# Kernel tuning notes

Measured on AMD Instinct MI355X. Metric: run time of the kernel, lower is better.

The kernel has to match this reference:

```python
import jax, jax.numpy as jnp
import numpy as np

B, T, H, IN = 256, 1024, 512, 1

def setup_inputs() -> dict:
    key = jax.random.key(0)
    ks = jax.random.split(key, 10)
    s = 1.0 / np.sqrt(H)
    return {
        "input": jax.random.normal(ks[0], (B, T), dtype=jnp.float32),
        "Wx0": jax.random.uniform(ks[1], (IN, 4 * H), jnp.float32, -s, s),
        "Wh0": jax.random.uniform(ks[2], (H, 4 * H), jnp.float32, -s, s),
        "b0": jax.random.uniform(ks[3], (4 * H,), jnp.float32, -s, s),
        "Wx1": jax.random.uniform(ks[4], (H, 4 * H), jnp.float32, -s, s),
        "Wh1": jax.random.uniform(ks[5], (H, 4 * H), jnp.float32, -s, s),
        "b1": jax.random.uniform(ks[6], (4 * H,), jnp.float32, -s, s),
        "Wf": jax.random.uniform(ks[7], (H, 1), jnp.float32, -s, s),
        "bf": jax.random.uniform(ks[8], (1,), jnp.float32, -s, s),
    }

def _lstm_layer(xs, Wx, Wh, b):
    # xs: [T, B, in] -> hs: [T, B, H]
    Bd = xs.shape[1]
    Hd = Wh.shape[0]
    h0 = jnp.zeros((Bd, Hd), xs.dtype)
    c0 = jnp.zeros((Bd, Hd), xs.dtype)
    def step(carry, x_t):
        h, c = carry
        g = x_t @ Wx + h @ Wh + b                     # [B, 4H]
        i, f, gg, o = jnp.split(g, 4, axis=-1)
        i = jax.nn.sigmoid(i)
        f = jax.nn.sigmoid(f)
        gg = jnp.tanh(gg)
        o = jax.nn.sigmoid(o)
        c_n = f * c + i * gg
        h_n = o * jnp.tanh(c_n)
        return (h_n, c_n), h_n
    _, hs = jax.lax.scan(step, (h0, c0), xs)
    return hs

def reference(input, Wx0, Wh0, b0, Wx1, Wh1, b1, Wf, bf):
    # input: [B, T] scalar sequence (input_size = 1)
    xs = input.T[:, :, None]                           # [T, B, 1]
    h1 = _lstm_layer(xs, Wx0, Wh0, b0)                 # [T, B, H]
    h2 = _lstm_layer(h1, Wx1, Wh1, b1)                 # [T, B, H]
    out = h2 @ Wf + bf                                 # [T, B, 1]
    return out[:, :, 0].T                              # [B, T]
```

## Files before the change

### kernel.cpp

```cpp
#include <hip/hip_runtime.h>


typedef _Float16 f16;
typedef _Float16 f16x8 __attribute__((ext_vector_type(8)));
typedef float f32x4 __attribute__((ext_vector_type(4)));
typedef unsigned long long u64;

#define NB 256
#define NT_ 1024
#define NH 512
#define RING 16
#define SLOT (NB * NH)

__device__ __forceinline__ float sigm(float x)  { return 1.0f / (1.0f + __expf(-x)); }
__device__ __forceinline__ float tanhx(float x) { return 2.0f / (1.0f + __expf(-2.0f * x)) - 1.0f; }

__device__ __forceinline__ void st8(unsigned short* p, u64 v) {
  __hip_atomic_store((u64*)p, v, __ATOMIC_RELAXED, __HIP_MEMORY_SCOPE_AGENT);
}
__device__ __forceinline__ void stf(unsigned* p, unsigned v) {
  __hip_atomic_store(p, v, __ATOMIC_RELAXED, __HIP_MEMORY_SCOPE_AGENT);
}
__device__ __forceinline__ unsigned ldf(const unsigned* p) {
  return __hip_atomic_load(p, __ATOMIC_RELAXED, __HIP_MEMORY_SCOPE_AGENT);
}
__device__ __forceinline__ unsigned pollr(const unsigned* a, unsigned thr) {
  unsigned v;
  for (;;) {
    v = ldf(a);
    if (!~__ballot(v >= thr)) break;
    __builtin_amdgcn_s_sleep(1);
  }
  asm volatile("" ::: "memory");
  return v;
}

__device__ __forceinline__ unsigned* PFL(unsigned* pf, int c, int j, int r) {
  return pf + (((c * 32 + j) * 4) + r) * 32;
}
__device__ __forceinline__ unsigned* QFL(unsigned* qf, int c, int j, int r) {
  return qf + (((c * 32 + j) * 4) + r) * 32;
}

__global__ void prep_xT(const float* __restrict__ inp, float* __restrict__ xT) {
  int g = blockIdx.x * 256 + threadIdx.x;
  int t = g >> 8, b = g & 255;
  xT[t * NB + b] = inp[b * NT_ + t];
}

__global__ void prep_w(const float* __restrict__ Wh0,
                       const float* __restrict__ Wx1,
                       const float* __restrict__ Wh1,
                       f16* __restrict__ dst) {
  int g = blockIdx.x * 256 + threadIdx.x;
  int mat = g >> 20;
  int r = g & 0xFFFFF;
  int j = r & 7, ln = (r >> 3) & 63, kt = (r >> 9) & 15;
  int cl = ln & 15, qd = ln >> 4;
  int k = kt * 32 + qd * 8 + j;
  int jt = (r >> 13) & 1, nh = (r >> 14) & 1, sl = (r >> 15) & 31;
  const float* W = (mat == 0) ? Wh0 : (mat == 1) ? Wx1 : Wh1;
  int gate = jt * 2 + (cl >> 3);
  int gcol = gate * 512 + sl * 16 + nh * 8 + (cl & 7);
  size_t di = (size_t)mat * 1048576 + (size_t)sl * 32768 +
              (((size_t)(nh * 2 + jt) * 16 + kt) * 64 + ln) * 8 + j;
  dst[di] = (f16)W[(size_t)k * 2048 + gcol];
}

__global__ void reduce_out(const float* __restrict__ part8,
                           const float* __restrict__ bfp,
                           float* __restrict__ out) {
  int g = blockIdx.x * 256 + threadIdx.x;
  float v = bfp[0];
#pragma unroll
  for (int j = 0; j < 8; ++j) v += part8[(size_t)j * (NB * NT_) + g];
  out[g] = v;
}

__global__ __launch_bounds__(256, 1) void lstm_main(
    const float* __restrict__ xT,
    const f16*  __restrict__ wsl,
    const float* __restrict__ wx0,
    const float* __restrict__ bias0,
    const float* __restrict__ bias1,
    const float* __restrict__ wf,
    unsigned short* p_hi, unsigned short* p_lo,
    unsigned short* q_hi, unsigned short* q_lo,
    unsigned int* pf,
    unsigned int* qf,
    float* part8)
{
  extern __shared__ char smem[];
  const int tid = threadIdx.x;
  const int wv = tid >> 6, ln = tid & 63;
  const int qd = ln >> 4, cl = ln & 15;
  const int bx = blockIdx.x;
  const int r8 = bx & 7, idx = bx >> 3;
  const bool isL0 = !(r8 & 1);
  const int c = r8 >> 1;
  const int sl = idx;
  const float LO = 1.0f / 1024.0f;
  const int u = cl & 7, g01 = cl >> 3;
  const bool hiH = (cl < 8);
  const int lr = wv * 16 + cl;

  if (isL0) {
    const int4* s0 = (const int4*)wsl + (size_t)sl * 4096;
    int4* d = (int4*)smem;
    for (int i = tid; i < 4096; i += 256) d[i] = s0[i];
  } else {
    const int4* s1 = (const int4*)wsl + 131072 + (size_t)sl * 4096;
    const int4* s2 = (const int4*)wsl + 262144 + (size_t)sl * 4096;
    int4* d = (int4*)smem;
    for (int i = tid; i < 4096; i += 256) { d[i] = s1[i]; d[4096 + i] = s2[i]; }
  }
  __syncthreads();

  if (isL0) {
    float w0a[2], w0b[2], b0a[2], b0b[2];
#pragma unroll
    for (int nh = 0; nh < 2; ++nh) {
      int base = sl * 16 + nh * 8 + u;
      w0a[nh] = wx0[g01 * 512 + base];
      b0a[nh] = bias0[g01 * 512 + base];
      w0b[nh] = wx0[(2 + g01) * 512 + base];
      b0b[nh] = bias0[(2 + g01) * 512 + base];
    }
    float cst[2][4] = {{0.f,0.f,0.f,0.f},{0.f,0.f,0.f,0.f}};
    const unsigned* pwa = (ln < 32) ? PFL(pf, c, ln, sl & 3)
                                    : QFL(qf, c, ln - 32, sl & 3);
    const f16x8* wl = (const f16x8*)smem;
    f16* sh  = (f16*)(smem + 65536);
    f16* slo = sh + 1024;

    for (int s = 0; s < NT_; ++s) {
      if ((s & (RING - 1)) == 0 && s) {
        __syncthreads();
        if (wv == 0)
          asm volatile("buffer_inv sc1\n\ts_waitcnt vmcnt(0)" ::: "memory");
        __syncthreads();
      }
      const int slot_r = (s + RING - 1) & (RING - 1);
      const int slot_w = s & (RING - 1);
      float4 xv = *(const float4*)(xT + s * NB + c * 64 + wv * 16 + qd * 4);
      if (s) {
        unsigned thr = (ln < 32) ? (unsigned)s
                                 : (s >= RING ? (unsigned)(s - RING + 1) : 0u);
        pollr(pwa, thr);
      }
      const f16* ah = (const f16*)p_hi + (size_t)slot_r * SLOT + (size_t)c * 32768 +
                      (qd >> 1) * 1024 + lr * 16 + (qd & 1) * 8;
      const f16* al = (const f16*)p_lo + (size_t)slot_r * SLOT + (size_t)c * 32768 +
                      (qd >> 1) * 1024 + lr * 16 + (qd & 1) * 8;
      f16x8 Ah[16], Al[16];
#pragma unroll
      for (int kt = 0; kt < 16; ++kt) {
        Ah[kt] = *(const f16x8*)(ah + kt * 2048);
        Al[kt] = *(const f16x8*)(al + kt * 2048);
      }
      f32x4 acc[4], accL[4];
#pragma unroll
      for (int t4 = 0; t4 < 4; ++t4) {
        acc[t4] = (f32x4){0.f,0.f,0.f,0.f};
        accL[t4] = (f32x4){0.f,0.f,0.f,0.f};
      }
#pragma unroll
      for (int kt = 0; kt < 16; ++kt) {
#pragma unroll
        for (int t4 = 0; t4 < 4; ++t4) {
          f16x8 bw = wl[(t4 * 16 + kt) * 64 + ln];
          acc[t4]  = __builtin_amdgcn_mfma_f32_16x16x32_f16(Ah[kt], bw, acc[t4], 0, 0, 0);
          accL[t4] = __builtin_amdgcn_mfma_f32_16x16x32_f16(Al[kt], bw, accL[t4], 0, 0, 0);
        }
      }
#pragma unroll
      for (int e = 0; e < 4; ++e) {
        float xe = (e == 0) ? xv.x : (e == 1) ? xv.y : (e == 2) ? xv.z : xv.w;
        int r = wv * 16 + qd * 4 + e;
#pragma unroll
        for (int nh = 0; nh < 2; ++nh) {
          float v0 = acc[nh*2+0][e] + accL[nh*2+0][e] * LO + xe * w0a[nh] + b0a[nh];
          float v1 = acc[nh*2+1][e] + accL[nh*2+1][e] * LO + xe * w0b[nh] + b0b[nh];
          float w0 = __shfl_xor(v0, 8, 16);
          float w1 = __shfl_xor(v1, 8, 16);
          float gi = hiH ? v0 : w0;
          float gf = hiH ? w0 : v0;
          float gg = hiH ? v1 : w1;
          float go = hiH ? w1 : v1;
          float ii = sigm(gi), ff = sigm(gf), tg = tanhx(gg), oo = sigm(go);
          cst[nh][e] = ff * cst[nh][e] + ii * tg;
          float h = oo * tanhx(cst[nh][e]);
          int su = r * 16 + nh * 8 + u;
          if (hiH) {
            sh[su] = (f16)h;
          } else {
            f16 hh = (f16)h;
            slo[su] = (f16)((h - (float)hh) * 1024.0f);
          }
        }
      }
      __syncthreads();
      {
        unsigned short* bh = p_hi + (size_t)slot_w * SLOT + (size_t)c * 32768 + (size_t)sl * 1024;
        unsigned short* bl = p_lo + (size_t)slot_w * SLOT + (size_t)c * 32768 + (size_t)sl * 1024;
#pragma unroll
        for (int i = tid; i < 512; i += 256) {
          int strm = i >> 8, pc = i & 255;
          const f16* src = (strm ? slo : sh) + pc * 4;
          st8((strm ? bl : bh) + pc * 4, *(const u64*)src);
        }
      }
      __syncthreads();
      if (tid < 4)
        stf(PFL(pf, c, sl, tid), (unsigned)(s + 1));
    }
  } else {
    float b1c0[2], b1c1[2], wfv[2];
#pragma unroll
    for (int nh = 0; nh < 2; ++nh) {
      int base = sl * 16 + nh * 8 + u;
      b1c0[nh] = bias1[g01 * 512 + base];
      b1c1[nh] = bias1[(2 + g01) * 512 + base];
      wfv[nh] = wf[base];
    }
    float cst[2][4] = {{0.f,0.f,0.f,0.f},{0.f,0.f,0.f,0.f}};
    const unsigned* a_init = (ln < 32) ? QFL(qf, c, ln, sl & 3)
                                       : PFL(pf, c, ln - 32, sl & 3);
    const unsigned* ppf = PFL(pf, c, ln & 31, (sl + (ln >> 5)) & 3);
    const f16x8* wx_ = (const f16x8*)smem;
    const f16x8* wh_ = (const f16x8*)(smem + 65536);
    f16* sh  = (f16*)(smem + 131072);
    f16* slo = sh + 1024;

    for (int s = 0; s < NT_; ++s) {
      if ((s & (RING - 1)) == 0 && s) {
        __syncthreads();
        if (wv == 0)
          asm volatile("buffer_inv sc1\n\ts_waitcnt vmcnt(0)" ::: "memory");
        __syncthreads();
      }
      const int slot_r = (s + RING - 1) & (RING - 1);
      const int slot_w = s & (RING - 1);
      bool early = false;
      if (s) {
        unsigned thr_i = (ln < 32) ? (unsigned)s : (unsigned)(s + 1);
        unsigned v = ldf(a_init);
        u64 bal = __ballot(v >= thr_i);
        while ((unsigned)bal != 0xFFFFFFFFu) {
          __builtin_amdgcn_s_sleep(1);
          v = ldf(a_init);
          bal = __ballot(v >= thr_i);
        }
        asm volatile("" ::: "memory");
        early = ((unsigned)(bal >> 32) == 0xFFFFFFFFu);
      }
      const f16* aqh = (const f16*)q_hi + (size_t)slot_r * SLOT + (size_t)c * 32768 +
                       (qd >> 1) * 1024 + lr * 16 + (qd & 1) * 8;
      const f16* aql = (const f16*)q_lo + (size_t)slot_r * SLOT + (size_t)c * 32768 +
                       (qd >> 1) * 1024 + lr * 16 + (qd & 1) * 8;
      f16x8 Aq[16][2];
#pragma unroll
      for (int kt = 0; kt < 16; ++kt) {
        Aq[kt][0] = *(const f16x8*)(aqh + kt * 2048);
        Aq[kt][1] = *(const f16x8*)(aql + kt * 2048);
      }
      const f16* aph = (const f16*)p_hi + (size_t)slot_w * SLOT + (size_t)c * 32768 +
                       (qd >> 1) * 1024 + lr * 16 + (qd & 1) * 8;
      const f16* apl = (const f16*)p_lo + (size_t)slot_w * SLOT + (size_t)c * 32768 +
                       (qd >> 1) * 1024 + lr * 16 + (qd & 1) * 8;
      f16x8 Ap[16][2];
      if (early) {
#pragma unroll
        for (int kt = 0; kt < 16; ++kt) {
          Ap[kt][0] = *(const f16x8*)(aph + kt * 2048);
          Ap[kt][1] = *(const f16x8*)(apl + kt * 2048);
        }
      }
      f32x4 acc[4], accL[4];
#pragma unroll
      for (int t4 = 0; t4 < 4; ++t4) {
        acc[t4] = (f32x4){0.f,0.f,0.f,0.f};
        accL[t4] = (f32x4){0.f,0.f,0.f,0.f};
      }
#pragma unroll
      for (int kt = 0; kt < 16; ++kt) {
#pragma unroll
        for (int t4 = 0; t4 < 4; ++t4) {
          f16x8 bw = wh_[(t4 * 16 + kt) * 64 + ln];
          acc[t4]  = __builtin_amdgcn_mfma_f32_16x16x32_f16(Aq[kt][0], bw, acc[t4], 0, 0, 0);
          accL[t4] = __builtin_amdgcn_mfma_f32_16x16x32_f16(Aq[kt][1], bw, accL[t4], 0, 0, 0);
        }
      }
      if (!early) {
        pollr(ppf, (unsigned)(s + 1));
#pragma unroll
        for (int kt = 0; kt < 16; ++kt) {
          Ap[kt][0] = *(const f16x8*)(aph + kt * 2048);
          Ap[kt][1] = *(const f16x8*)(apl + kt * 2048);
        }
      }
#pragma unroll
      for (int kt = 0; kt < 16; ++kt) {
#pragma unroll
        for (int t4 = 0; t4 < 4; ++t4) {
          f16x8 bw = wx_[(t4 * 16 + kt) * 64 + ln];
          acc[t4]  = __builtin_amdgcn_mfma_f32_16x16x32_f16(Ap[kt][0], bw, acc[t4], 0, 0, 0);
          accL[t4] = __builtin_amdgcn_mfma_f32_16x16x32_f16(Ap[kt][1], bw, accL[t4], 0, 0, 0);
        }
      }
      float po[4];
#pragma unroll
      for (int e = 0; e < 4; ++e) {
        po[e] = 0.0f;
#pragma unroll
        for (int nh = 0; nh < 2; ++nh) {
          float v0 = acc[nh*2+0][e] + accL[nh*2+0][e] * LO + b1c0[nh];
          float v1 = acc[nh*2+1][e] + accL[nh*2+1][e] * LO + b1c1[nh];
          float w0 = __shfl_xor(v0, 8, 16);
          float w1 = __shfl_xor(v1, 8, 16);
          float gi = hiH ? v0 : w0;
          float gf = hiH ? w0 : v0;
          float gg = hiH ? v1 : w1;
          float go = hiH ? w1 : v1;
          float ii = sigm(gi), ff = sigm(gf), tg = tanhx(gg), oo = sigm(go);
          cst[nh][e] = ff * cst[nh][e] + ii * tg;
          float h = oo * tanhx(cst[nh][e]);
          int su = (wv * 16 + qd * 4 + e) * 16 + nh * 8 + u;
          if (hiH) {
            sh[su] = (f16)h;
          } else {
            f16 hh = (f16)h;
            slo[su] = (f16)((h - (float)hh) * 1024.0f);
          }
          po[e] += hiH ? wfv[nh] * h : 0.0f;
        }
      }
      __syncthreads();
      {
        unsigned short* bhq = q_hi + (size_t)slot_w * SLOT + (size_t)c * 32768 + (size_t)sl * 1024;
        unsigned short* blq = q_lo + (size_t)slot_w * SLOT + (size_t)c * 32768 + (size_t)sl * 1024;
#pragma unroll
        for (int i = tid; i < 512; i += 256) {
          int strm = i >> 8, pc = i & 255;
          const f16* src = (strm ? slo : sh) + pc * 4;
          st8((strm ? blq : bhq) + pc * 4, *(const u64*)src);
        }
      }
      __syncthreads();
      if (tid < 4)
        stf(QFL(qf, c, sl, tid), (unsigned)(s + 1));
#pragma unroll
      for (int e = 0; e < 4; ++e) {
        float r = po[e];
#pragma unroll
        for (int m = 1; m < 16; m <<= 1) r += __shfl_xor(r, m, 16);
        if (cl == 0)
          atomicAdd(part8 + (size_t)(sl & 7) * (NB * NT_) +
                        (size_t)(c * 64 + wv * 16 + qd * 4 + e) * NT_ + s, r);
      }
    }
  }
}

extern "C" void kernel_launch(void* const* d_in, const int* in_sizes, int n_in,
                              void* d_out, int out_size, void* d_ws, size_t ws_size,
                              hipStream_t stream) {
  (void)in_sizes; (void)n_in; (void)out_size; (void)ws_size;
  const float* inp = (const float*)d_in[0];
  const float* Wx0 = (const float*)d_in[1];
  const float* Wh0 = (const float*)d_in[2];
  const float* b0  = (const float*)d_in[3];
  const float* Wx1 = (const float*)d_in[4];
  const float* Wh1 = (const float*)d_in[5];
  const float* b1  = (const float*)d_in[6];
  const float* Wf  = (const float*)d_in[7];
  const float* bf  = (const float*)d_in[8];

  const size_t MB = 1u << 20;
  const size_t OFF_W    = 0;
  const size_t OFF_XT   = 6 * MB;
  const size_t OFF_PHI  = 7 * MB;
  const size_t OFF_PLO  = 11 * MB;
  const size_t OFF_QHI  = 15 * MB;
  const size_t OFF_QLO  = 19 * MB;
  const size_t OFF_PART = 23 * MB;
  const size_t OFF_CTR  = 31 * MB;

  char* ws = (char*)d_ws;
  f16* wsl = (f16*)(ws + OFF_W);
  float* xT = (float*)(ws + OFF_XT);
  unsigned short* phi = (unsigned short*)(ws + OFF_PHI);
  unsigned short* plo = (unsigned short*)(ws + OFF_PLO);
  unsigned short* qhi = (unsigned short*)(ws + OFF_QHI);
  unsigned short* qlo = (unsigned short*)(ws + OFF_QLO);
  float* part8 = (float*)(ws + OFF_PART);
  unsigned int* pfl = (unsigned int*)(ws + OFF_CTR);
  unsigned int* qfl = pfl + 16384;
  float* out = (float*)d_out;

  (void)hipFuncSetAttribute((const void*)lstm_main,
                            hipFuncAttributeMaxDynamicSharedMemorySize, 135168);

  (void)hipMemsetAsync(ws + OFF_PHI, 0, (OFF_CTR + 131072) - OFF_PHI, stream);

  prep_xT<<<1024, 256, 0, stream>>>(inp, xT);
  prep_w<<<12288, 256, 0, stream>>>(Wh0, Wx1, Wh1, wsl);

  lstm_main<<<256, 256, 135168, stream>>>(xT, wsl, Wx0, b0, b1, Wf,
                                          phi, plo, qhi, qlo, pfl, qfl, part8);

  reduce_out<<<1024, 256, 0, stream>>>(part8, bf, out);
}
```

Before: 9.664 ms.

## Replace block barriers with per-wave flag publishing in LSTM step loop

Each wave now writes its own 16-row slice of h to a private LDS region, stores it straight to the global ring and publishes a per-wave ready flag. This replaces the two __syncthreads per timestep and the barriers around the ring-wrap cache invalidate. Consumers poll the per-wave flag that matches their own wave index. The aim is to cut intra-block barrier stalls on the serial recurrence critical path. In exchange it relies on the s_waitcnt ordering and on each wave's slice being self-contained, which makes the memory ordering more fragile.

```diff
diff --git a/kernel.cpp b/kernel.cpp
--- a/kernel.cpp
+++ b/kernel.cpp
@@ -35,11 +35,11 @@
   return v;
 }
 
-__device__ __forceinline__ unsigned* PFL(unsigned* pf, int c, int j, int r) {
-  return pf + (((c * 32 + j) * 4) + r) * 32;
-}
-__device__ __forceinline__ unsigned* QFL(unsigned* qf, int c, int j, int r) {
-  return qf + (((c * 32 + j) * 4) + r) * 32;
+__device__ __forceinline__ unsigned* PFL(unsigned* pf, int c, int j, int w) {
+  return pf + (((c * 32 + j) * 4) + w) * 32;
+}
+__device__ __forceinline__ unsigned* QFL(unsigned* qf, int c, int j, int w) {
+  return qf + (((c * 32 + j) * 4) + w) * 32;
 }
 
 __global__ void prep_xT(const float* __restrict__ inp, float* __restrict__ xT) {
@@ -127,19 +127,15 @@
       b0b[nh] = bias0[(2 + g01) * 512 + base];
     }
     float cst[2][4] = {{0.f,0.f,0.f,0.f},{0.f,0.f,0.f,0.f}};
-    const unsigned* pwa = (ln < 32) ? PFL(pf, c, ln, sl & 3)
-                                    : QFL(qf, c, ln - 32, sl & 3);
+    const unsigned* pwa = (ln < 32) ? PFL(pf, c, ln, wv)
+                                    : QFL(qf, c, ln - 32, wv);
     const f16x8* wl = (const f16x8*)smem;
-    f16* sh  = (f16*)(smem + 65536);
-    f16* slo = sh + 1024;
+    f16* shW  = (f16*)(smem + 65536) + wv * 256;
+    f16* sloW = (f16*)(smem + 65536) + 1024 + wv * 256;
 
     for (int s = 0; s < NT_; ++s) {
-      if ((s & (RING - 1)) == 0 && s) {
-        __syncthreads();
-        if (wv == 0)
-          asm volatile("buffer_inv sc1\n\ts_waitcnt vmcnt(0)" ::: "memory");
-        __syncthreads();
-      }
+      if ((s & (RING - 1)) == 0 && s)
+        asm volatile("buffer_inv sc1\n\ts_waitcnt vmcnt(0)" ::: "memory");
       const int slot_r = (s + RING - 1) & (RING - 1);
       const int slot_w = s & (RING - 1);
       float4 xv = *(const float4*)(xT + s * NB + c * 64 + wv * 16 + qd * 4);
@@ -176,7 +172,6 @@
 #pragma unroll
       for (int e = 0; e < 4; ++e) {
         float xe = (e == 0) ? xv.x : (e == 1) ? xv.y : (e == 2) ? xv.z : xv.w;
-        int r = wv * 16 + qd * 4 + e;
 #pragma unroll
         for (int nh = 0; nh < 2; ++nh) {
           float v0 = acc[nh*2+0][e] + accL[nh*2+0][e] * LO + xe * w0a[nh] + b0a[nh];
@@ -190,29 +185,24 @@
           float ii = sigm(gi), ff = sigm(gf), tg = tanhx(gg), oo = sigm(go);
           cst[nh][e] = ff * cst[nh][e] + ii * tg;
           float h = oo * tanhx(cst[nh][e]);
-          int su = r * 16 + nh * 8 + u;
+          int su = (qd * 4 + e) * 16 + nh * 8 + u;
           if (hiH) {
-            sh[su] = (f16)h;
+            shW[su] = (f16)h;
           } else {
             f16 hh = (f16)h;
-            slo[su] = (f16)((h - (float)hh) * 1024.0f);
+            sloW[su] = (f16)((h - (float)hh) * 1024.0f);
           }
         }
       }
-      __syncthreads();
+      asm volatile("s_waitcnt lgkmcnt(0)" ::: "memory");
       {
-        unsigned short* bh = p_hi + (size_t)slot_w * SLOT + (size_t)c * 32768 + (size_t)sl * 1024;
-        unsigned short* bl = p_lo + (size_t)slot_w * SLOT + (size_t)c * 32768 + (size_t)sl * 1024;
-#pragma unroll
-        for (int i = tid; i < 512; i += 256) {
-          int strm = i >> 8, pc = i & 255;
-          const f16* src = (strm ? slo : sh) + pc * 4;
-          st8((strm ? bl : bh) + pc * 4, *(const u64*)src);
-        }
-      }
-      __syncthreads();
-      if (tid < 4)
-        stf(PFL(pf, c, sl, tid), (unsigned)(s + 1));
+        size_t boff = (size_t)slot_w * SLOT + (size_t)c * 32768 +
+                      (size_t)sl * 1024 + wv * 256;
+        st8(p_hi + boff + ln * 4, *(const u64*)(shW + ln * 4));
+        st8(p_lo + boff + ln * 4, *(const u64*)(sloW + ln * 4));
+      }
+      asm volatile("s_waitcnt vmcnt(0)" ::: "memory");
+      if (ln == 0) stf(PFL(pf, c, sl, wv), (unsigned)(s + 1));
     }
   } else {
     float b1c0[2], b1c1[2], wfv[2];
@@ -224,21 +214,17 @@
       wfv[nh] = wf[base];
     }
     float cst[2][4] = {{0.f,0.f,0.f,0.f},{0.f,0.f,0.f,0.f}};
-    const unsigned* a_init = (ln < 32) ? QFL(qf, c, ln, sl & 3)
-                                       : PFL(pf, c, ln - 32, sl & 3);
-    const unsigned* ppf = PFL(pf, c, ln & 31, (sl + (ln >> 5)) & 3);
+    const unsigned* a_init = (ln < 32) ? QFL(qf, c, ln, wv)
+                                       : PFL(pf, c, ln - 32, wv);
+    const unsigned* ppf = PFL(pf, c, ln & 31, wv);
     const f16x8* wx_ = (const f16x8*)smem;
     const f16x8* wh_ = (const f16x8*)(smem + 65536);
-    f16* sh  = (f16*)(smem + 131072);
-    f16* slo = sh + 1024;
+    f16* shW  = (f16*)(smem + 131072) + wv * 256;
+    f16* sloW = (f16*)(smem + 131072) + 1024 + wv * 256;
 
     for (int s = 0; s < NT_; ++s) {
-      if ((s & (RING - 1)) == 0 && s) {
-        __syncthreads();
-        if (wv == 0)
-          asm volatile("buffer_inv sc1\n\ts_waitcnt vmcnt(0)" ::: "memory");
-        __syncthreads();
-      }
+      if ((s & (RING - 1)) == 0 && s)
+        asm volatile("buffer_inv sc1\n\ts_waitcnt vmcnt(0)" ::: "memory");
       const int slot_r = (s + RING - 1) & (RING - 1);
       const int slot_w = s & (RING - 1);
       bool early = false;
@@ -325,30 +311,25 @@
           float ii = sigm(gi), ff = sigm(gf), tg = tanhx(gg), oo = sigm(go);
           cst[nh][e] = ff * cst[nh][e] + ii * tg;
           float h = oo * tanhx(cst[nh][e]);
-          int su = (wv * 16 + qd * 4 + e) * 16 + nh * 8 + u;
+          int su = (qd * 4 + e) * 16 + nh * 8 + u;
           if (hiH) {
-            sh[su] = (f16)h;
+            shW[su] = (f16)h;
           } else {
             f16 hh = (f16)h;
-            slo[su] = (f16)((h - (float)hh) * 1024.0f);
+            sloW[su] = (f16)((h - (float)hh) * 1024.0f);
           }
           po[e] += hiH ? wfv[nh] * h : 0.0f;
         }
       }
-      __syncthreads();
+      asm volatile("s_waitcnt lgkmcnt(0)" ::: "memory");
       {
-        unsigned short* bhq = q_hi + (size_t)slot_w * SLOT + (size_t)c * 32768 + (size_t)sl * 1024;
-        unsigned short* blq = q_lo + (size_t)slot_w * SLOT + (size_t)c * 32768 + (size_t)sl * 1024;
-#pragma unroll
-        for (int i = tid; i < 512; i += 256) {
-          int strm = i >> 8, pc = i & 255;
-          const f16* src = (strm ? slo : sh) + pc * 4;
-          st8((strm ? blq : bhq) + pc * 4, *(const u64*)src);
-        }
-      }
-      __syncthreads();
-      if (tid < 4)
-        stf(QFL(qf, c, sl, tid), (unsigned)(s + 1));
+        size_t boff = (size_t)slot_w * SLOT + (size_t)c * 32768 +
+                      (size_t)sl * 1024 + wv * 256;
+        st8(q_hi + boff + ln * 4, *(const u64*)(shW + ln * 4));
+        st8(q_lo + boff + ln * 4, *(const u64*)(sloW + ln * 4));
+      }
+      asm volatile("s_waitcnt vmcnt(0)" ::: "memory");
+      if (ln == 0) stf(QFL(qf, c, sl, wv), (unsigned)(s + 1));
 #pragma unroll
       for (int e = 0; e < 4; ++e) {
         float r = po[e];
```

Result: slower. 10.39 ms (+7.5%).

## Embed parity bits in hidden-state data to replace flag-based step synchronization

Applied to the files above, without the earlier changes.

Each stored f16 value, both the hi and lo halves, now has its low mantissa bit replaced by a ring-epoch parity bit. Consumers poll the data itself with atomic loads until every word shows the expected parity, which removes the per-step flag stores, the extra barrier and the periodic cache-invalidate. Backpressure is reduced to a per-block progress counter checked every 8 steps, and the shared staging buffers are double-buffered. In exchange it loses one mantissa bit of precision in both halves and repeatedly re-reads the full operand tile while spinning.

```diff
diff --git a/kernel.cpp b/kernel.cpp
--- a/kernel.cpp
+++ b/kernel.cpp
@@ -5,18 +5,24 @@
 typedef _Float16 f16x8 __attribute__((ext_vector_type(8)));
 typedef float f32x4 __attribute__((ext_vector_type(4)));
 typedef unsigned long long u64;
+typedef unsigned long long u64x2 __attribute__((ext_vector_type(2)));
+typedef unsigned short u16;
 
 #define NB 256
 #define NT_ 1024
 #define NH 512
 #define RING 16
 #define SLOT (NB * NH)
+#define PMASK 0x0001000100010001ull
 
 __device__ __forceinline__ float sigm(float x)  { return 1.0f / (1.0f + __expf(-x)); }
 __device__ __forceinline__ float tanhx(float x) { return 2.0f / (1.0f + __expf(-2.0f * x)) - 1.0f; }
 
-__device__ __forceinline__ void st8(unsigned short* p, u64 v) {
+__device__ __forceinline__ void st8(u16* p, u64 v) {
   __hip_atomic_store((u64*)p, v, __ATOMIC_RELAXED, __HIP_MEMORY_SCOPE_AGENT);
+}
+__device__ __forceinline__ u64 ld8a(const u16* p) {
+  return __hip_atomic_load((const u64*)p, __ATOMIC_RELAXED, __HIP_MEMORY_SCOPE_AGENT);
 }
 __device__ __forceinline__ void stf(unsigned* p, unsigned v) {
   __hip_atomic_store(p, v, __ATOMIC_RELAXED, __HIP_MEMORY_SCOPE_AGENT);
@@ -24,22 +30,17 @@
 __device__ __forceinline__ unsigned ldf(const unsigned* p) {
   return __hip_atomic_load(p, __ATOMIC_RELAXED, __HIP_MEMORY_SCOPE_AGENT);
 }
-__device__ __forceinline__ unsigned pollr(const unsigned* a, unsigned thr) {
-  unsigned v;
+__device__ __forceinline__ void pollr(const unsigned* a, unsigned thr) {
   for (;;) {
-    v = ldf(a);
+    unsigned v = ldf(a);
     if (!~__ballot(v >= thr)) break;
     __builtin_amdgcn_s_sleep(1);
   }
   asm volatile("" ::: "memory");
-  return v;
-}
-
-__device__ __forceinline__ unsigned* PFL(unsigned* pf, int c, int j, int r) {
-  return pf + (((c * 32 + j) * 4) + r) * 32;
-}
-__device__ __forceinline__ unsigned* QFL(unsigned* qf, int c, int j, int r) {
-  return qf + (((c * 32 + j) * 4) + r) * 32;
+}
+__device__ __forceinline__ f16x8 frag(u64 w0, u64 w1) {
+  u64x2 t; t.x = w0; t.y = w1;
+  return __builtin_bit_cast(f16x8, t);
 }
 
 __global__ void prep_xT(const float* __restrict__ inp, float* __restrict__ xT) {
@@ -84,10 +85,9 @@
     const float* __restrict__ bias0,
     const float* __restrict__ bias1,
     const float* __restrict__ wf,
-    unsigned short* p_hi, unsigned short* p_lo,
-    unsigned short* q_hi, unsigned short* q_lo,
-    unsigned int* pf,
-    unsigned int* qf,
+    u16* p_hi, u16* p_lo,
+    u16* q_hi, u16* q_lo,
+    unsigned int* prog,
     float* part8)
 {
   extern __shared__ char smem[];
@@ -116,6 +116,8 @@
   }
   __syncthreads();
 
+  unsigned* progc = prog + c * 32 * 32;
+
   if (isL0) {
     float w0a[2], w0b[2], b0a[2], b0b[2];
 #pragma unroll
@@ -127,52 +129,58 @@
       b0b[nh] = bias0[(2 + g01) * 512 + base];
     }
     float cst[2][4] = {{0.f,0.f,0.f,0.f},{0.f,0.f,0.f,0.f}};
-    const unsigned* pwa = (ln < 32) ? PFL(pf, c, ln, sl & 3)
-                                    : QFL(qf, c, ln - 32, sl & 3);
+    const unsigned* pga = progc + (ln & 31) * 32;
     const f16x8* wl = (const f16x8*)smem;
-    f16* sh  = (f16*)(smem + 65536);
-    f16* slo = sh + 1024;
 
     for (int s = 0; s < NT_; ++s) {
-      if ((s & (RING - 1)) == 0 && s) {
-        __syncthreads();
-        if (wv == 0)
-          asm volatile("buffer_inv sc1\n\ts_waitcnt vmcnt(0)" ::: "memory");
-        __syncthreads();
-      }
+      if (s >= 16 && (s & 7) == 0) pollr(pga, (unsigned)(s - 8));
       const int slot_r = (s + RING - 1) & (RING - 1);
       const int slot_w = s & (RING - 1);
       float4 xv = *(const float4*)(xT + s * NB + c * 64 + wv * 16 + qd * 4);
-      if (s) {
-        unsigned thr = (ln < 32) ? (unsigned)s
-                                 : (s >= RING ? (unsigned)(s - RING + 1) : 0u);
-        pollr(pwa, thr);
-      }
-      const f16* ah = (const f16*)p_hi + (size_t)slot_r * SLOT + (size_t)c * 32768 +
-                      (qd >> 1) * 1024 + lr * 16 + (qd & 1) * 8;
-      const f16* al = (const f16*)p_lo + (size_t)slot_r * SLOT + (size_t)c * 32768 +
-                      (qd >> 1) * 1024 + lr * 16 + (qd & 1) * 8;
-      f16x8 Ah[16], Al[16];
-#pragma unroll
-      for (int kt = 0; kt < 16; ++kt) {
-        Ah[kt] = *(const f16x8*)(ah + kt * 2048);
-        Al[kt] = *(const f16x8*)(al + kt * 2048);
-      }
       f32x4 acc[4], accL[4];
 #pragma unroll
       for (int t4 = 0; t4 < 4; ++t4) {
         acc[t4] = (f32x4){0.f,0.f,0.f,0.f};
         accL[t4] = (f32x4){0.f,0.f,0.f,0.f};
       }
-#pragma unroll
-      for (int kt = 0; kt < 16; ++kt) {
-#pragma unroll
-        for (int t4 = 0; t4 < 4; ++t4) {
-          f16x8 bw = wl[(t4 * 16 + kt) * 64 + ln];
-          acc[t4]  = __builtin_amdgcn_mfma_f32_16x16x32_f16(Ah[kt], bw, acc[t4], 0, 0, 0);
-          accL[t4] = __builtin_amdgcn_mfma_f32_16x16x32_f16(Al[kt], bw, accL[t4], 0, 0, 0);
-        }
-      }
+      if (s) {
+        const u16* ah = (const u16*)p_hi + (size_t)slot_r * SLOT + (size_t)c * 32768 +
+                        (qd >> 1) * 1024 + lr * 16 + (qd & 1) * 8;
+        const u16* al = (const u16*)p_lo + (size_t)slot_r * SLOT + (size_t)c * 32768 +
+                        (qd >> 1) * 1024 + lr * 16 + (qd & 1) * 8;
+        const u64 want = (((s - 1) >> 4) & 1) ? PMASK : 0ull;
+        u64 wh_a[32], wl_a[32];
+        for (;;) {
+#pragma unroll
+          for (int kt = 0; kt < 16; ++kt) {
+            wh_a[2*kt]   = ld8a(ah + kt * 2048);
+            wh_a[2*kt+1] = ld8a(ah + kt * 2048 + 4);
+            wl_a[2*kt]   = ld8a(al + kt * 2048);
+            wl_a[2*kt+1] = ld8a(al + kt * 2048 + 4);
+          }
+          bool ok = true;
+#pragma unroll
+          for (int i = 0; i < 32; ++i)
+            ok &= ((wh_a[i] & PMASK) == want) & ((wl_a[i] & PMASK) == want);
+          if (!~__ballot(ok)) break;
+          __builtin_amdgcn_s_sleep(1);
+        }
+        asm volatile("" ::: "memory");
+#pragma unroll
+        for (int kt = 0; kt < 16; ++kt) {
+          f16x8 Ah = frag(wh_a[2*kt], wh_a[2*kt+1]);
+          f16x8 Al = frag(wl_a[2*kt], wl_a[2*kt+1]);
+#pragma unroll
+          for (int t4 = 0; t4 < 4; ++t4) {
+            f16x8 bw = wl[(t4 * 16 + kt) * 64 + ln];
+            acc[t4]  = __builtin_amdgcn_mfma_f32_16x16x32_f16(Ah, bw, acc[t4], 0, 0, 0);
+            accL[t4] = __builtin_amdgcn_mfma_f32_16x16x32_f16(Al, bw, accL[t4], 0, 0, 0);
+          }
+        }
+      }
+      u16* shp = (u16*)(smem + 65536) + (s & 1) * 2048;
+      u16* slp = shp + 1024;
+      const u16 P = (u16)((s >> 4) & 1);
 #pragma unroll
       for (int e = 0; e < 4; ++e) {
         float xe = (e == 0) ? xv.x : (e == 1) ? xv.y : (e == 2) ? xv.z : xv.w;
@@ -190,29 +198,28 @@
           float ii = sigm(gi), ff = sigm(gf), tg = tanhx(gg), oo = sigm(go);
           cst[nh][e] = ff * cst[nh][e] + ii * tg;
           float h = oo * tanhx(cst[nh][e]);
+          u16 hb = (u16)((__builtin_bit_cast(u16, (f16)h) & 0xFFFEu) | P);
           int su = r * 16 + nh * 8 + u;
           if (hiH) {
-            sh[su] = (f16)h;
+            shp[su] = hb;
           } else {
-            f16 hh = (f16)h;
-            slo[su] = (f16)((h - (float)hh) * 1024.0f);
+            f16 hf = __builtin_bit_cast(f16, hb);
+            f16 l16 = (f16)((h - (float)hf) * 1024.0f);
+            slp[su] = (u16)((__builtin_bit_cast(u16, l16) & 0xFFFEu) | P);
           }
         }
       }
       __syncthreads();
       {
-        unsigned short* bh = p_hi + (size_t)slot_w * SLOT + (size_t)c * 32768 + (size_t)sl * 1024;
-        unsigned short* bl = p_lo + (size_t)slot_w * SLOT + (size_t)c * 32768 + (size_t)sl * 1024;
+        u16* bh = p_hi + (size_t)slot_w * SLOT + (size_t)c * 32768 + (size_t)sl * 1024;
+        u16* bl = p_lo + (size_t)slot_w * SLOT + (size_t)c * 32768 + (size_t)sl * 1024;
 #pragma unroll
         for (int i = tid; i < 512; i += 256) {
           int strm = i >> 8, pc = i & 255;
-          const f16* src = (strm ? slo : sh) + pc * 4;
+          const u16* src = (strm ? slp : shp) + pc * 4;
           st8((strm ? bl : bh) + pc * 4, *(const u64*)src);
         }
       }
-      __syncthreads();
-      if (tid < 4)
-        stf(PFL(pf, c, sl, tid), (unsigned)(s + 1));
     }
   } else {
     float b1c0[2], b1c1[2], wfv[2];
@@ -224,94 +231,97 @@
       wfv[nh] = wf[base];
     }
     float cst[2][4] = {{0.f,0.f,0.f,0.f},{0.f,0.f,0.f,0.f}};
-    const unsigned* a_init = (ln < 32) ? QFL(qf, c, ln, sl & 3)
-                                       : PFL(pf, c, ln - 32, sl & 3);
-    const unsigned* ppf = PFL(pf, c, ln & 31, (sl + (ln >> 5)) & 3);
+    unsigned* prog_me = progc + sl * 32;
     const f16x8* wx_ = (const f16x8*)smem;
     const f16x8* wh_ = (const f16x8*)(smem + 65536);
-    f16* sh  = (f16*)(smem + 131072);
-    f16* slo = sh + 1024;
-
-    for (int s = 0; s < NT_; ++s) {
-      if ((s & (RING - 1)) == 0 && s) {
-        __syncthreads();
-        if (wv == 0)
-          asm volatile("buffer_inv sc1\n\ts_waitcnt vmcnt(0)" ::: "memory");
-        __syncthreads();
-      }
-      const int slot_r = (s + RING - 1) & (RING - 1);
-      const int slot_w = s & (RING - 1);
-      bool early = false;
-      if (s) {
-        unsigned thr_i = (ln < 32) ? (unsigned)s : (unsigned)(s + 1);
-        unsigned v = ldf(a_init);
-        u64 bal = __ballot(v >= thr_i);
-        while ((unsigned)bal != 0xFFFFFFFFu) {
-          __builtin_amdgcn_s_sleep(1);
-          v = ldf(a_init);
-          bal = __ballot(v >= thr_i);
-        }
-        asm volatile("" ::: "memory");
-        early = ((unsigned)(bal >> 32) == 0xFFFFFFFFu);
-      }
-      const f16* aqh = (const f16*)q_hi + (size_t)slot_r * SLOT + (size_t)c * 32768 +
-                       (qd >> 1) * 1024 + lr * 16 + (qd & 1) * 8;
-      const f16* aql = (const f16*)q_lo + (size_t)slot_r * SLOT + (size_t)c * 32768 +
-                       (qd >> 1) * 1024 + lr * 16 + (qd & 1) * 8;
-      f16x8 Aq[16][2];
-#pragma unroll
-      for (int kt = 0; kt < 16; ++kt) {
-        Aq[kt][0] = *(const f16x8*)(aqh + kt * 2048);
-        Aq[kt][1] = *(const f16x8*)(aql + kt * 2048);
-      }
-      const f16* aph = (const f16*)p_hi + (size_t)slot_w * SLOT + (size_t)c * 32768 +
-                       (qd >> 1) * 1024 + lr * 16 + (qd & 1) * 8;
-      const f16* apl = (const f16*)p_lo + (size_t)slot_w * SLOT + (size_t)c * 32768 +
-                       (qd >> 1) * 1024 + lr * 16 + (qd & 1) * 8;
-      f16x8 Ap[16][2];
-      if (early) {
-#pragma unroll
-        for (int kt = 0; kt < 16; ++kt) {
-          Ap[kt][0] = *(const f16x8*)(aph + kt * 2048);
-          Ap[kt][1] = *(const f16x8*)(apl + kt * 2048);
-        }
-      }
+
+    for (int t = 0; t < NT_; ++t) {
+      const int slot_r = (t + RING - 1) & (RING - 1);
+      const int slot_w = t & (RING - 1);
       f32x4 acc[4], accL[4];
 #pragma unroll
       for (int t4 = 0; t4 < 4; ++t4) {
         acc[t4] = (f32x4){0.f,0.f,0.f,0.f};
         accL[t4] = (f32x4){0.f,0.f,0.f,0.f};
       }
-#pragma unroll
-      for (int kt = 0; kt < 16; ++kt) {
-#pragma unroll
-        for (int t4 = 0; t4 < 4; ++t4) {
-          f16x8 bw = wh_[(t4 * 16 + kt) * 64 + ln];
-          acc[t4]  = __builtin_amdgcn_mfma_f32_16x16x32_f16(Aq[kt][0], bw, acc[t4], 0, 0, 0);
-          accL[t4] = __builtin_amdgcn_mfma_f32_16x16x32_f16(Aq[kt][1], bw, accL[t4], 0, 0, 0);
-        }
-      }
-      if (!early) {
-        pollr(ppf, (unsigned)(s + 1));
+      if (t) {
+        const u16* aqh = (const u16*)q_hi + (size_t)slot_r * SLOT + (size_t)c * 32768 +
+                         (qd >> 1) * 1024 + lr * 16 + (qd & 1) * 8;
+        const u16* aql = (const u16*)q_lo + (size_t)slot_r * SLOT + (size_t)c * 32768 +
+                         (qd >> 1) * 1024 + lr * 16 + (qd & 1) * 8;
+        const u64 want = (((t - 1) >> 4) & 1) ? PMASK : 0ull;
+        u64 wh_a[32], wl_a[32];
+        for (;;) {
+#pragma unroll
+          for (int kt = 0; kt < 16; ++kt) {
+            wh_a[2*kt]   = ld8a(aqh + kt * 2048);
+            wh_a[2*kt+1] = ld8a(aqh + kt * 2048 + 4);
+            wl_a[2*kt]   = ld8a(aql + kt * 2048);
+            wl_a[2*kt+1] = ld8a(aql + kt * 2048 + 4);
+          }
+          bool ok = true;
+#pragma unroll
+          for (int i = 0; i < 32; ++i)
+            ok &= ((wh_a[i] & PMASK) == want) & ((wl_a[i] & PMASK) == want);
+          if (!~__ballot(ok)) break;
+          __builtin_amdgcn_s_sleep(1);
+        }
+        asm volatile("" ::: "memory");
 #pragma unroll
         for (int kt = 0; kt < 16; ++kt) {
-          Ap[kt][0] = *(const f16x8*)(aph + kt * 2048);
-          Ap[kt][1] = *(const f16x8*)(apl + kt * 2048);
-        }
-      }
-#pragma unroll
-      for (int kt = 0; kt < 16; ++kt) {
-#pragma unroll
-        for (int t4 = 0; t4 < 4; ++t4) {
-          f16x8 bw = wx_[(t4 * 16 + kt) * 64 + ln];
-          acc[t4]  = __builtin_amdgcn_mfma_f32_16x16x32_f16(Ap[kt][0], bw, acc[t4], 0, 0, 0);
-          accL[t4] = __builtin_amdgcn_mfma_f32_16x16x32_f16(Ap[kt][1], bw, accL[t4], 0, 0, 0);
-        }
-      }
+          f16x8 Ah = frag(wh_a[2*kt], wh_a[2*kt+1]);
+          f16x8 Al = frag(wl_a[2*kt], wl_a[2*kt+1]);
+#pragma unroll
+          for (int t4 = 0; t4 < 4; ++t4) {
+            f16x8 bw = wh_[(t4 * 16 + kt) * 64 + ln];
+            acc[t4]  = __builtin_amdgcn_mfma_f32_16x16x32_f16(Ah, bw, acc[t4], 0, 0, 0);
+            accL[t4] = __builtin_amdgcn_mfma_f32_16x16x32_f16(Al, bw, accL[t4], 0, 0, 0);
+          }
+        }
+      }
+      {
+        const u16* aph = (const u16*)p_hi + (size_t)slot_w * SLOT + (size_t)c * 32768 +
+                         (qd >> 1) * 1024 + lr * 16 + (qd & 1) * 8;
+        const u16* apl = (const u16*)p_lo + (size_t)slot_w * SLOT + (size_t)c * 32768 +
+                         (qd >> 1) * 1024 + lr * 16 + (qd & 1) * 8;
+        const u64 want = ((t >> 4) & 1) ? PMASK : 0ull;
+        u64 wh_a[32], wl_a[32];
+        for (;;) {
+#pragma unroll
+          for (int kt = 0; kt < 16; ++kt) {
+            wh_a[2*kt]   = ld8a(aph + kt * 2048);
+            wh_a[2*kt+1] = ld8a(aph + kt * 2048 + 4);
+            wl_a[2*kt]   = ld8a(apl + kt * 2048);
+            wl_a[2*kt+1] = ld8a(apl + kt * 2048 + 4);
+          }
+          bool ok = true;
+#pragma unroll
+          for (int i = 0; i < 32; ++i)
+            ok &= ((wh_a[i] & PMASK) == want) & ((wl_a[i] & PMASK) == want);
+          if (!~__ballot(ok)) break;
+          __builtin_amdgcn_s_sleep(1);
+        }
+        asm volatile("" ::: "memory");
+#pragma unroll
+        for (int kt = 0; kt < 16; ++kt) {
+          f16x8 Ah = frag(wh_a[2*kt], wh_a[2*kt+1]);
+          f16x8 Al = frag(wl_a[2*kt], wl_a[2*kt+1]);
+#pragma unroll
+          for (int t4 = 0; t4 < 4; ++t4) {
+            f16x8 bw = wx_[(t4 * 16 + kt) * 64 + ln];
+            acc[t4]  = __builtin_amdgcn_mfma_f32_16x16x32_f16(Ah, bw, acc[t4], 0, 0, 0);
+            accL[t4] = __builtin_amdgcn_mfma_f32_16x16x32_f16(Al, bw, accL[t4], 0, 0, 0);
+          }
+        }
+      }
+      u16* shq = (u16*)(smem + 131072) + (t & 1) * 2048;
+      u16* slq = shq + 1024;
+      const u16 P = (u16)((t >> 4) & 1);
       float po[4];
 #pragma unroll
       for (int e = 0; e < 4; ++e) {
         po[e] = 0.0f;
+        int r = wv * 16 + qd * 4 + e;
 #pragma unroll
         for (int nh = 0; nh < 2; ++nh) {
           float v0 = acc[nh*2+0][e] + accL[nh*2+0][e] * LO + b1c0[nh];
@@ -325,30 +335,30 @@
           float ii = sigm(gi), ff = sigm(gf), tg = tanhx(gg), oo = sigm(go);
           cst[nh][e] = ff * cst[nh][e] + ii * tg;
           float h = oo * tanhx(cst[nh][e]);
-          int su = (wv * 16 + qd * 4 + e) * 16 + nh * 8 + u;
+          u16 hb = (u16)((__builtin_bit_cast(u16, (f16)h) & 0xFFFEu) | P);
+          int su = r * 16 + nh * 8 + u;
           if (hiH) {
-            sh[su] = (f16)h;
+            shq[su] = hb;
           } else {
-            f16 hh = (f16)h;
-            slo[su] = (f16)((h - (float)hh) * 1024.0f);
+            f16 hf = __builtin_bit_cast(f16, hb);
+            f16 l16 = (f16)((h - (float)hf) * 1024.0f);
+            slq[su] = (u16)((__builtin_bit_cast(u16, l16) & 0xFFFEu) | P);
           }
           po[e] += hiH ? wfv[nh] * h : 0.0f;
         }
       }
       __syncthreads();
+      if (tid == 0) stf(prog_me, (unsigned)(t + 1));
       {
-        unsigned short* bhq = q_hi + (size_t)slot_w * SLOT + (size_t)c * 32768 + (size_t)sl * 1024;
-        unsigned short* blq = q_lo + (size_t)slot_w * SLOT + (size_t)c * 32768 + (size_t)sl * 1024;
+        u16* bh = q_hi + (size_t)slot_w * SLOT + (size_t)c * 32768 + (size_t)sl * 1024;
+        u16* bl = q_lo + (size_t)slot_w * SLOT + (size_t)c * 32768 + (size_t)sl * 1024;
 #pragma unroll
         for (int i = tid; i < 512; i += 256) {
           int strm = i >> 8, pc = i & 255;
-          const f16* src = (strm ? slo : sh) + pc * 4;
-          st8((strm ? blq : bhq) + pc * 4, *(const u64*)src);
-        }
-      }
-      __syncthreads();
-      if (tid < 4)
-        stf(QFL(qf, c, sl, tid), (unsigned)(s + 1));
+          const u16* src = (strm ? slq : shq) + pc * 4;
+          st8((strm ? bl : bh) + pc * 4, *(const u64*)src);
+        }
+      }
 #pragma unroll
       for (int e = 0; e < 4; ++e) {
         float r = po[e];
@@ -356,7 +366,7 @@
         for (int m = 1; m < 16; m <<= 1) r += __shfl_xor(r, m, 16);
         if (cl == 0)
           atomicAdd(part8 + (size_t)(sl & 7) * (NB * NT_) +
-                        (size_t)(c * 64 + wv * 16 + qd * 4 + e) * NT_ + s, r);
+                        (size_t)(c * 64 + wv * 16 + qd * 4 + e) * NT_ + t, r);
       }
     }
   }
@@ -384,30 +394,30 @@
   const size_t OFF_QHI  = 15 * MB;
   const size_t OFF_QLO  = 19 * MB;
   const size_t OFF_PART = 23 * MB;
-  const size_t OFF_CTR  = 31 * MB;
+  const size_t OFF_PROG = 31 * MB;
 
   char* ws = (char*)d_ws;
   f16* wsl = (f16*)(ws + OFF_W);
   float* xT = (float*)(ws + OFF_XT);
-  unsigned short* phi = (unsigned short*)(ws + OFF_PHI);
-  unsigned short* plo = (unsigned short*)(ws + OFF_PLO);
-  unsigned short* qhi = (unsigned short*)(ws + OFF_QHI);
-  unsigned short* qlo = (unsigned short*)(ws + OFF_QLO);
+  u16* phi = (u16*)(ws + OFF_PHI);
+  u16* plo = (u16*)(ws + OFF_PLO);
+  u16* qhi = (u16*)(ws + OFF_QHI);
+  u16* qlo = (u16*)(ws + OFF_QLO);
   float* part8 = (float*)(ws + OFF_PART);
-  unsigned int* pfl = (unsigned int*)(ws + OFF_CTR);
-  unsigned int* qfl = pfl + 16384;
+  unsigned int* prog = (unsigned int*)(ws + OFF_PROG);
   float* out = (float*)d_out;
 
   (void)hipFuncSetAttribute((const void*)lstm_main,
-                            hipFuncAttributeMaxDynamicSharedMemorySize, 135168);
-
-  (void)hipMemsetAsync(ws + OFF_PHI, 0, (OFF_CTR + 131072) - OFF_PHI, stream);
+                            hipFuncAttributeMaxDynamicSharedMemorySize, 139264);
+
+  (void)hipMemsetAsync(ws + OFF_PHI, 0xFF, 16 * MB, stream);
+  (void)hipMemsetAsync(ws + OFF_PART, 0, 8 * MB + 16384, stream);
 
   prep_xT<<<1024, 256, 0, stream>>>(inp, xT);
   prep_w<<<12288, 256, 0, stream>>>(Wh0, Wx1, Wh1, wsl);
 
-  lstm_main<<<256, 256, 135168, stream>>>(xT, wsl, Wx0, b0, b1, Wf,
-                                          phi, plo, qhi, qlo, pfl, qfl, part8);
+  lstm_main<<<256, 256, 139264, stream>>>(xT, wsl, Wx0, b0, b1, Wf,
+                                          phi, plo, qhi, qlo, prog, part8);
 
   reduce_out<<<1024, 256, 0, stream>>>(part8, bf, out);
 }
```

After: 9.879 ms. 2.2% more time.
